# Performance work log

Hardware: AMD Instinct MI355X
Metric: run time of the kernel (lower is better)

The kernel has to match this reference:

```python
import jax, jax.numpy as jnp
import numpy as np

D_MODEL = 1024
N_HEADS = 16
D_K = D_MODEL // N_HEADS


def setup_inputs() -> dict:
    key = jax.random.key(0)
    k1, k2, k3 = jax.random.split(key, 3)
    x = jax.random.normal(k1, (4, 2048, D_MODEL), dtype=jnp.float32)
    # torch nn.Linear(d_model, 3*d_model, bias=False): y = x @ W.T, W: [3D, D].
    # We store transposed weights [D, 3D] so y = x @ W_attn (same math).
    scale = 1.0 / np.sqrt(D_MODEL)
    W_attn = jax.random.uniform(k2, (D_MODEL, 3 * D_MODEL), dtype=jnp.float32, minval=-scale, maxval=scale)
    W_proj = jax.random.uniform(k3, (D_MODEL, D_MODEL), dtype=jnp.float32, minval=-scale, maxval=scale)
    return {"x": x, "W_attn": W_attn, "W_proj": W_proj}


def reference(x, W_attn, W_proj):
    B, S, D = x.shape
    qkv = x @ W_attn                       # [B, S, 3D]
    q, k, v = jnp.split(qkv, 3, axis=-1)   # each [B, S, D]
    # [B, S, D] -> [B, H, S, d_k]
    def heads(t):
        return t.reshape(B, S, N_HEADS, D_K).transpose(0, 2, 1, 3)
    q, k, v = heads(q), heads(k), heads(v)
    scores = jnp.einsum('bhqd,bhkd->bhqk', q, k) / jnp.sqrt(jnp.float32(D_K))
    weights = jax.nn.softmax(scores, axis=-1)
    attn = jnp.einsum('bhqk,bhkd->bhqd', weights, v)  # [B, H, S, d_k]
    attn = attn.transpose(0, 2, 1, 3).reshape(B, S, D)
    return attn @ W_proj
```

## Files before the change

### kernel.cpp

```cpp
#include <hip/hip_runtime.h>
#include <hip/hip_bf16.h>

#define D_MODEL 1024
#define N_HEADS 16
#define SEQ     2048
#define BATCH   4
#define CSC     (0.125f * 1.44269504f)

typedef __attribute__((ext_vector_type(8))) short short8;
typedef __attribute__((ext_vector_type(4))) float f32x4;

__device__ __forceinline__ ushort f2bf(float v) {
    __hip_bfloat16 b = __float2bfloat16(v);
    return __builtin_bit_cast(ushort, b);
}
__device__ __forceinline__ f32x4 mfma16(short8 a, short8 b, f32x4 c) {
    return __builtin_amdgcn_mfma_f32_16x16x32_bf16(a, b, c, 0, 0, 0);
}
__device__ __forceinline__ void gload_lds16(const ushort* g, ushort* l) {
    __builtin_amdgcn_global_load_lds(
        (const __attribute__((address_space(1))) unsigned int*)g,
        (__attribute__((address_space(3))) unsigned int*)l, 16, 0, 0);
}

__global__ __launch_bounds__(256) void prep_k(const float* __restrict__ x,
                                              const float* __restrict__ Wa,
                                              const float* __restrict__ Wp,
                                              ushort* __restrict__ xh,
                                              ushort* __restrict__ WaT,
                                              ushort* __restrict__ WpT) {
    const int id = blockIdx.x;
    const int t = threadIdx.x;
    if (id < 2048) {
        const float4* x4 = (const float4*)x;
        ushort4* xh4 = (ushort4*)xh;
        const int n4 = BATCH * SEQ * D_MODEL / 4;
        for (int i = id * 256 + t; i < n4; i += 2048 * 256) {
            float4 v = x4[i];
            ushort4 hv;
            hv.x = f2bf(v.x);
            hv.y = f2bf(v.y);
            hv.z = f2bf(v.z);
            hv.w = f2bf(v.w);
            xh4[i] = hv;
        }
    } else {
        __shared__ float tile[32][33];
        const float* W;
        ushort* WT;
        int N, tid, scaleQ;
        if (id < 2048 + 3072) { tid = id - 2048; W = Wa; WT = WaT; N = 3072; scaleQ = 1; }
        else                  { tid = id - 5120; W = Wp; WT = WpT; N = 1024; scaleQ = 0; }
        const int nb = (tid % (N / 32)) * 32, kb = (tid / (N / 32)) * 32;
        const int tx = t & 31, ty = t >> 5;
#pragma unroll
        for (int i = 0; i < 4; ++i)
            tile[ty + 8 * i][tx] = W[(size_t)(kb + ty + 8 * i) * N + nb + tx];
        __syncthreads();
#pragma unroll
        for (int i = 0; i < 4; ++i) {
            int n = nb + ty + 8 * i;
            float v = tile[tx][ty + 8 * i];
            if (scaleQ && n < 1024) v *= CSC;
            WT[(size_t)n * 1024 + kb + tx] = f2bf(v);
        }
    }
}

__global__ __launch_bounds__(256) void transpose_v_k(const ushort* __restrict__ qkv_h,
                                                     ushort* __restrict__ vT_h) {
    __shared__ ushort th[64][68];
    const int st = blockIdx.x, h = blockIdx.y, b = blockIdx.z;
    const int t = threadIdx.x;
    const int s0 = st * 64;
    {
        int s = t >> 2, dc = (t & 3) * 16;
        const size_t src = ((size_t)(b * SEQ + s0 + s)) * 3072 + 2048 + h * 64 + dc;
        *(uint4*)&th[s][dc]     = *(const uint4*)&qkv_h[src];
        *(uint4*)&th[s][dc + 8] = *(const uint4*)&qkv_h[src + 8];
    }
    __syncthreads();
    {
        int d = t >> 2, sc = (t & 3) * 16;
        ushort bufh[16];
#pragma unroll
        for (int j = 0; j < 16; ++j) bufh[j] = th[sc + j][d];
        const size_t dst = ((size_t)((b * 16 + h) * 64 + d)) * SEQ + s0 + sc;
        *(uint4*)&vT_h[dst]     = *(uint4*)&bufh[0];
        *(uint4*)&vT_h[dst + 8] = *(uint4*)&bufh[8];
    }
}

template <int OUT_SPLIT>
__global__ __launch_bounds__(256) void gemm_k(
    const ushort* __restrict__ Ah, int lda, int aoff,
    const ushort* __restrict__ BhT,
    ushort* __restrict__ Ch, float* __restrict__ Cf,
    int ldc, int coff, int K) {
    __shared__ __align__(16) ushort lds[2][2][4096];
    const int t = threadIdx.x;
    const int lane = t & 63, wid = t >> 6;
    const int wm = (wid >> 1) * 64, wn = (wid & 1) * 64;

    const int gx = gridDim.x;
    const int nwg = gx * gridDim.y;
    const int flat = blockIdx.y * gx + blockIdx.x;
    const int swzid = (flat & 7) * (nwg >> 3) + (flat >> 3);
    const int row0 = (swzid / gx) * 128, col0 = (swzid % gx) * 128;

    f32x4 acc[4][4];
#pragma unroll
    for (int i = 0; i < 4; ++i)
#pragma unroll
        for (int j = 0; j < 4; ++j) acc[i][j] = f32x4{0.f, 0.f, 0.f, 0.f};

    const int r_loc = lane >> 2;
    const int c_src = (lane & 3) ^ ((lane >> 3) & 3);
    const int swz = ((lane & 15) >> 1) & 3;
    const int ch = (((lane >> 4) ^ swz) * 8);
    const int rA = wm + (lane & 15);
    const int rB = wn + (lane & 15);

    auto stage = [&](int buf, int kk) {
#pragma unroll
        for (int ic = 0; ic < 4; ++ic) {
            const int c = wid * 4 + ic;
            const int tile = c >> 3, chi = c & 7;
            const ushort* s = tile ? BhT : Ah;
            const int sr = tile ? col0 : row0;
            const int sl = tile ? K : lda;
            const int so = tile ? 0 : aoff;
            const ushort* gp =
                s + (size_t)(sr + chi * 16 + r_loc) * sl + so + kk + c_src * 8;
            gload_lds16(gp, &lds[buf][tile][chi * 512 + 0]);
        }
    };

    stage(0, 0);
    for (int k0 = 0; k0 < K; k0 += 32) {
        const int cur = (k0 >> 5) & 1;
        if (k0 + 32 < K) {
            stage(cur ^ 1, k0 + 32);
            asm volatile("s_waitcnt vmcnt(4)" ::: "memory");
        } else {
            asm volatile("s_waitcnt vmcnt(0)" ::: "memory");
        }
        __builtin_amdgcn_s_barrier();
        __builtin_amdgcn_sched_barrier(0);

        short8 ah[4], bh[4];
#pragma unroll
        for (int f = 0; f < 4; ++f) {
            ah[f] = *(const short8*)&lds[cur][0][(rA + f * 16) * 32 + ch];
            bh[f] = *(const short8*)&lds[cur][1][(rB + f * 16) * 32 + ch];
        }
        __builtin_amdgcn_s_setprio(1);
#pragma unroll
        for (int i = 0; i < 4; ++i)
#pragma unroll
            for (int j = 0; j < 4; ++j) acc[i][j] = mfma16(ah[i], bh[j], acc[i][j]);
        __builtin_amdgcn_s_setprio(0);
        asm volatile("s_waitcnt lgkmcnt(0)" ::: "memory");
        __builtin_amdgcn_s_barrier();
        __builtin_amdgcn_sched_barrier(0);
    }
#pragma unroll
    for (int i = 0; i < 4; ++i)
#pragma unroll
        for (int j = 0; j < 4; ++j)
#pragma unroll
            for (int r = 0; r < 4; ++r) {
                int row = row0 + wm + i * 16 + (lane >> 4) * 4 + r;
                int col = col0 + wn + j * 16 + (lane & 15);
                float v = acc[i][j][r];
                if (OUT_SPLIT) {
                    Ch[(size_t)row * ldc + coff + col] = f2bf(v);
                } else {
                    Cf[(size_t)row * ldc + coff + col] = v;
                }
            }
}

__global__ __launch_bounds__(512) void flash_mfma(
    const ushort* __restrict__ qkv_h, const ushort* __restrict__ vT_h,
    ushort* __restrict__ attn_h) {
    const int id = blockIdx.x;
    const int bh = id & 63, qt = id >> 6;
    const int h = bh & 15, b = bh >> 4;
    const int t = threadIdx.x, lane = t & 63, wid = t >> 6;
    const int q = lane & 15, g = lane >> 4;
    const int qs7 = q & 7;

    __shared__ __align__(16) ushort Kb[2][4096];
    __shared__ __align__(16) ushort Vb[2][4096];
    __shared__ __align__(16) ushort Pb[8][1024];

    const size_t tokbase = (size_t)b * SEQ;
    const int q0 = qt * 128;
    const int kv_r = lane >> 3;
    const int kv_csrc = (lane & 7) ^ ((lane >> 3) & 7);
    const size_t vbase = ((size_t)(b * 16 + h) * 64) * SEQ;

    ushort* KQ = &Kb[0][0];
#pragma unroll
    for (int is = 0; is < 2; ++is) {
        int ci = wid * 2 + is;
        const ushort* gq =
            qkv_h + (tokbase + q0 + ci * 8 + kv_r) * 3072 + h * 64 + kv_csrc * 8;
        gload_lds16(gq, KQ + ci * 512);
    }
    __syncthreads();
    const int ck0 = (g ^ qs7) * 8;
    const int ck1 = ((g + 4) ^ qs7) * 8;
    short8 qh[2];
    {
        const int row = wid * 16 + q;
        qh[0] = *(const short8*)&KQ[row * 64 + ck0];
        qh[1] = *(const short8*)&KQ[row * 64 + ck1];
    }
    __syncthreads();

    const int qck0 = q * 64 + ck0;
    const int qck1 = q * 64 + ck1;
    ushort* Pw = &Pb[wid][0];
    const int pw0 = q * 64 + (((g >> 1) + 0) ^ qs7) * 8 + (g & 1) * 4;
    const int pw1 = q * 64 + (((g >> 1) + 2) ^ qs7) * 8 + (g & 1) * 4;
    const int pw2 = q * 64 + (((g >> 1) + 4) ^ qs7) * 8 + (g & 1) * 4;
    const int pw3 = q * 64 + (((g >> 1) + 6) ^ qs7) * 8 + (g & 1) * 4;

    auto stage = [&](int buf, int kv0) {
        if (wid < 4) {
            const ushort* gsrc =
                qkv_h + (tokbase + kv0 + wid * 16) * 3072 + 1024 + h * 64;
            ushort* dst = &Kb[buf][wid * 1024];
#pragma unroll
            for (int is = 0; is < 2; ++is)
                gload_lds16(gsrc + (size_t)(is * 8 + kv_r) * 3072 + kv_csrc * 8,
                            dst + is * 512);
        } else {
            const ushort* gsrc = vT_h + vbase + (size_t)((wid - 4) * 16) * SEQ + kv0;
            ushort* dst = &Vb[buf][(wid - 4) * 1024];
#pragma unroll
            for (int is = 0; is < 2; ++is)
                gload_lds16(gsrc + (size_t)(is * 8 + kv_r) * SEQ + kv_csrc * 8,
                            dst + is * 512);
        }
    };

    stage(0, 0);

    float l_ = 0.f;
    f32x4 o[4];
#pragma unroll
    for (int i = 0; i < 4; ++i) o[i] = f32x4{0.f, 0.f, 0.f, 0.f};

    auto body = [&](int cur) {
        const ushort* Kc = &Kb[cur][0];
        const ushort* Vc = &Vb[cur][0];

        f32x4 s[4];
#pragma unroll
        for (int j = 0; j < 4; ++j) s[j] = f32x4{0.f, 0.f, 0.f, 0.f};
        __builtin_amdgcn_s_setprio(1);
#pragma unroll
        for (int j = 0; j < 4; ++j) {
            short8 kh0 = *(const short8*)&Kc[j * 1024 + qck0];
            s[j] = mfma16(kh0, qh[0], s[j]);
            short8 kh1 = *(const short8*)&Kc[j * 1024 + qck1];
            s[j] = mfma16(kh1, qh[1], s[j]);
        }
        __builtin_amdgcn_s_setprio(0);

        float rs = 0.f;
#pragma unroll
        for (int j = 0; j < 4; ++j) {
            ushort4 hv;
            float p0 = __builtin_exp2f(s[j][0]);
            float p1 = __builtin_exp2f(s[j][1]);
            float p2 = __builtin_exp2f(s[j][2]);
            float p3 = __builtin_exp2f(s[j][3]);
            rs += (p0 + p1) + (p2 + p3);
            hv.x = f2bf(p0);
            hv.y = f2bf(p1);
            hv.z = f2bf(p2);
            hv.w = f2bf(p3);
            const int off = (j == 0) ? pw0 : (j == 1) ? pw1 : (j == 2) ? pw2 : pw3;
            *(ushort4*)&Pw[off] = hv;
        }
        l_ += rs;
        asm volatile("s_waitcnt lgkmcnt(0)" ::: "memory");
        __builtin_amdgcn_sched_barrier(0);

        __builtin_amdgcn_s_setprio(1);
#pragma unroll
        for (int ks = 0; ks < 2; ++ks) {
            short8 pa = *(const short8*)&Pw[ks ? qck1 : qck0];
#pragma unroll
            for (int jp = 0; jp < 4; ++jp) {
                short8 vh = *(const short8*)&Vc[jp * 1024 + (ks ? qck1 : qck0)];
                o[jp] = mfma16(pa, vh, o[jp]);
            }
        }
        __builtin_amdgcn_s_setprio(0);

        asm volatile("s_waitcnt lgkmcnt(0)" ::: "memory");
        __builtin_amdgcn_s_barrier();
        __builtin_amdgcn_sched_barrier(0);
    };

    for (int kt2 = 0; kt2 < SEQ / 128; ++kt2) {
        stage(1, (kt2 * 2 + 1) * 64);
        asm volatile("s_waitcnt vmcnt(2)" ::: "memory");
        __builtin_amdgcn_s_barrier();
        __builtin_amdgcn_sched_barrier(0);
        body(0);
        if (kt2 < SEQ / 128 - 1) {
            stage(0, (kt2 * 2 + 2) * 64);
            asm volatile("s_waitcnt vmcnt(2)" ::: "memory");
        } else {
            asm volatile("s_waitcnt vmcnt(0)" ::: "memory");
        }
        __builtin_amdgcn_s_barrier();
        __builtin_amdgcn_sched_barrier(0);
        body(1);
    }

    l_ += __shfl_xor(l_, 16);
    l_ += __shfl_xor(l_, 32);
    float inv = 1.f / l_;
#pragma unroll
    for (int r = 0; r < 4; ++r) {
        float invr = __shfl(inv, (g << 2) + r);
        int tok = q0 + wid * 16 + g * 4 + r;
        size_t rowb = (tokbase + tok) * 3072;
#pragma unroll
        for (int jp = 0; jp < 4; ++jp) {
            int col = h * 64 + jp * 16 + q;
            attn_h[rowb + col] = f2bf(o[jp][r] * invr);
        }
    }
}


extern "C" void kernel_launch(void* const* d_in, const int* in_sizes, int n_in,
                              void* d_out, int out_size, void* d_ws, size_t ws_size,
                              hipStream_t stream) {
    const float* x      = (const float*)d_in[0];
    const float* W_attn = (const float*)d_in[1];
    const float* W_proj = (const float*)d_in[2];

    const int M = BATCH * SEQ;

    ushort* qkv_h = (ushort*)d_ws;
    ushort* WaT   = qkv_h + (size_t)M * 3072;
    ushort* WpT   = WaT + (size_t)3072 * 1024;
    ushort* vT_h  = WpT + (size_t)1024 * 1024;

    ushort* xh = (ushort*)d_out;

    prep_k<<<dim3(6144), 256, 0, stream>>>(x, W_attn, W_proj, xh, WaT, WpT);
    gemm_k<1><<<dim3(24, 64), 256, 0, stream>>>(xh, 1024, 0, WaT,
                                                qkv_h, nullptr, 3072, 0, 1024);
    transpose_v_k<<<dim3(32, 16, 4), 256, 0, stream>>>(qkv_h, vT_h);
    flash_mfma<<<dim3(1024), 512, 0, stream>>>(qkv_h, vT_h, qkv_h + 2048);
    gemm_k<0><<<dim3(8, 64), 256, 0, stream>>>(qkv_h, 3072, 2048, WpT,
                                               nullptr, (float*)d_out, 1024, 0,
                                               1024);
}
```

Baseline: 217.3 us.

## Keep softmax P in registers by permuting V^T layout to match MFMA fragments

Removes the per-wave LDS round trip for the probability tile P in the flash attention loop. The exp results are packed straight into the MFMA A-operand registers. To keep P·V correct, the V transpose kernel now writes V^T with a permuted key ordering so the B operand matches the register layout of P. This drops the LDS stores, the waitcnt and the 16KB Pb buffer, at the cost of a less coalesced, ushort4-granular store pattern in the transpose kernel.

```diff
diff --git a/kernel.cpp b/kernel.cpp
--- a/kernel.cpp
+++ b/kernel.cpp
@@ -82,12 +82,17 @@
     __syncthreads();
     {
         int d = t >> 2, sc = (t & 3) * 16;
-        ushort bufh[16];
-#pragma unroll
-        for (int j = 0; j < 16; ++j) bufh[j] = th[sc + j][d];
-        const size_t dst = ((size_t)((b * 16 + h) * 64 + d)) * SEQ + s0 + sc;
-        *(uint4*)&vT_h[dst]     = *(uint4*)&bufh[0];
-        *(uint4*)&vT_h[dst + 8] = *(uint4*)&bufh[8];
+        const int c_off = ((sc & 16) ? 4 : 0) + ((sc & 32) ? 32 : 0);
+        const size_t dstbase = ((size_t)((b * 16 + h) * 64 + d)) * SEQ + s0;
+#pragma unroll
+        for (int jj = 0; jj < 4; ++jj) {
+            ushort4 v;
+            v.x = th[sc + 4 * jj + 0][d];
+            v.y = th[sc + 4 * jj + 1][d];
+            v.z = th[sc + 4 * jj + 2][d];
+            v.w = th[sc + 4 * jj + 3][d];
+            *(ushort4*)&vT_h[dstbase + 8 * jj + c_off] = v;
+        }
     }
 }
 
@@ -193,7 +198,6 @@
 
     __shared__ __align__(16) ushort Kb[2][4096];
     __shared__ __align__(16) ushort Vb[2][4096];
-    __shared__ __align__(16) ushort Pb[8][1024];
 
     const size_t tokbase = (size_t)b * SEQ;
     const int q0 = qt * 128;
@@ -222,11 +226,6 @@
 
     const int qck0 = q * 64 + ck0;
     const int qck1 = q * 64 + ck1;
-    ushort* Pw = &Pb[wid][0];
-    const int pw0 = q * 64 + (((g >> 1) + 0) ^ qs7) * 8 + (g & 1) * 4;
-    const int pw1 = q * 64 + (((g >> 1) + 2) ^ qs7) * 8 + (g & 1) * 4;
-    const int pw2 = q * 64 + (((g >> 1) + 4) ^ qs7) * 8 + (g & 1) * 4;
-    const int pw3 = q * 64 + (((g >> 1) + 6) ^ qs7) * 8 + (g & 1) * 4;
 
     auto stage = [&](int buf, int kv0) {
         if (wid < 4) {
@@ -272,33 +271,28 @@
         __builtin_amdgcn_s_setprio(0);
 
         float rs = 0.f;
+        short8 pa[2];
 #pragma unroll
         for (int j = 0; j < 4; ++j) {
-            ushort4 hv;
             float p0 = __builtin_exp2f(s[j][0]);
             float p1 = __builtin_exp2f(s[j][1]);
             float p2 = __builtin_exp2f(s[j][2]);
             float p3 = __builtin_exp2f(s[j][3]);
             rs += (p0 + p1) + (p2 + p3);
-            hv.x = f2bf(p0);
-            hv.y = f2bf(p1);
-            hv.z = f2bf(p2);
-            hv.w = f2bf(p3);
-            const int off = (j == 0) ? pw0 : (j == 1) ? pw1 : (j == 2) ? pw2 : pw3;
-            *(ushort4*)&Pw[off] = hv;
+            pa[j >> 1][(j & 1) * 4 + 0] = (short)f2bf(p0);
+            pa[j >> 1][(j & 1) * 4 + 1] = (short)f2bf(p1);
+            pa[j >> 1][(j & 1) * 4 + 2] = (short)f2bf(p2);
+            pa[j >> 1][(j & 1) * 4 + 3] = (short)f2bf(p3);
         }
         l_ += rs;
-        asm volatile("s_waitcnt lgkmcnt(0)" ::: "memory");
-        __builtin_amdgcn_sched_barrier(0);
 
         __builtin_amdgcn_s_setprio(1);
 #pragma unroll
         for (int ks = 0; ks < 2; ++ks) {
-            short8 pa = *(const short8*)&Pw[ks ? qck1 : qck0];
 #pragma unroll
             for (int jp = 0; jp < 4; ++jp) {
                 short8 vh = *(const short8*)&Vc[jp * 1024 + (ks ? qck1 : qck0)];
-                o[jp] = mfma16(pa, vh, o[jp]);
+                o[jp] = mfma16(pa[ks], vh, o[jp]);
             }
         }
         __builtin_amdgcn_s_setprio(0);
```

Measured after the change: 212.9 us. 2.0% less time.
